# Performance work log

Measured on AMD Instinct MI355X. Metric: run time of the kernel, lower is better.

## Reference

```python
import jax, jax.numpy as jnp
import numpy as np

SCALES = (8, 16, 32)  # matches init kwarg scale=[8,16,32]


def _pairwise_dist(x):
    # Euclidean cdist via the norm trick; clamp for numerical safety.
    sq = jnp.sum(x * x, axis=1)
    d2 = sq[:, None] + sq[None, :] - 2.0 * (x @ x.T)
    return jnp.sqrt(jnp.maximum(d2, 0.0))


def setup_inputs() -> dict:
    key = jax.random.key(0)
    k1, k2 = jax.random.split(key)
    N, D = 8192, 256
    feats_c_norm = jax.random.normal(k1, (N, D), dtype=jnp.float32)
    point_c_norm = jax.random.normal(k2, (N, 3), dtype=jnp.float32)
    f_masks = jnp.ones((N,), dtype=bool)  # all valid -> masked gather is identity (static shapes)
    return {"feats_c_norm": feats_c_norm, "point_c_norm": point_c_norm, "f_masks": f_masks}


def reference(feats_c_norm, point_c_norm, f_masks):
    # f_masks is all-True here, so feats_c_norm[f_indices] == feats_c_norm (identity).
    N = feats_c_norm.shape[0]
    dists = _pairwise_dist(point_c_norm)                     # [N, N]
    kmax = min(max(SCALES), N - 1) + 1
    # top_k of -dists gives the kmax smallest distances, sorted ascending,
    # so slicing idx[:, 1:s+1] reproduces per-scale topk(largest=False) exactly.
    _, idx = jax.lax.top_k(-dists, kmax)                     # [N, kmax] int32
    outs = [feats_c_norm]                                    # key 0 in the original dict
    for s in SCALES:
        s = min(s, N - 1)
        neighbor_feats = feats_c_norm[idx[:, 1:s + 1]]       # [N, s, D]
        outs.append(neighbor_feats.reshape(N, -1))           # [N, s*D]
    return tuple(outs)
```

## Files before the change

### kernel.cpp

```cpp
#include <hip/hip_runtime.h>

#define NPTS 8192
#define KSEL 33
#define SCAP 512

typedef float vf4 __attribute__((ext_vector_type(4)));

__global__ __launch_bounds__(256) void prep_kernel(const float* __restrict__ pts,
                                                   float4* __restrict__ pts4) {
#pragma clang fp contract(off)
    const int j = blockIdx.x * 256 + threadIdx.x;
    const float x = pts[j * 3 + 0];
    const float y = pts[j * 3 + 1];
    const float z = pts[j * 3 + 2];
    const float sq = (x * x + y * y) + z * z;
    pts4[j] = make_float4(x, y, z, sq);
}

__global__ __launch_bounds__(256, 4) void knn_fused_kernel(const float4* __restrict__ pts4,
                                                           const float* __restrict__ feats,
                                                           float* __restrict__ out) {
#pragma clang fp contract(off)
    const int i = blockIdx.x;
    const int tid = threadIdx.x;
    const int lane = tid & 63;
    const int wv = tid >> 6;

    __shared__ unsigned red[4];
    __shared__ int sh_cnt;
    __shared__ unsigned long long S[SCAP];
    __shared__ unsigned jlist[32];

    const float4 pi = pts4[i];

    unsigned d[32];
    unsigned m1 = 0xFFFFFFFFu, m2 = 0xFFFFFFFFu;
#pragma unroll
    for (int t = 0; t < 32; ++t) {
        const int j = tid + t * 256;
        const float4 pj = pts4[j];
        const float dot = __builtin_fmaf(pi.z, pj.z, __builtin_fmaf(pi.y, pj.y, pi.x * pj.x));
        const float d2 = (pi.w + pj.w) - (2.0f * dot);
        const unsigned db = __float_as_uint(fmaxf(d2, 0.0f));
        d[t] = db;
        const unsigned mx = db > m1 ? db : m1;
        m1 = db < m1 ? db : m1;
        m2 = mx < m2 ? mx : m2;
    }
    if (tid == 0) sh_cnt = 0;

    unsigned blo = 0u, bhi = 0x7F800000u;
    while (blo < bhi) {
        const unsigned mid = (blo + bhi) >> 1;
        const int cnt = __popcll(__ballot(m1 <= mid)) + __popcll(__ballot(m2 <= mid));
        if (cnt >= KSEL) bhi = mid; else blo = mid + 1u;
    }
    if (lane == 0) red[wv] = bhi;
    __syncthreads();
    unsigned T = red[0];
    T = red[1] < T ? red[1] : T;
    T = red[2] < T ? red[2] : T;
    T = red[3] < T ? red[3] : T;

    const float s = sqrtf(__uint_as_float(T));
    const float snx = __uint_as_float(__float_as_uint(s) + 1u);
    const unsigned T2 = __float_as_uint(__fmul_rn(snx, snx)) + 2u;

    int n = 0;
#pragma unroll
    for (int t = 0; t < 32; ++t) n += (d[t] <= T2) ? 1 : 0;

    int incl = n;
#pragma unroll
    for (int sh = 1; sh < 64; sh <<= 1) {
        const int o = __shfl_up(incl, sh, 64);
        if (lane >= sh) incl += o;
    }
    int base = 0;
    if (lane == 63) base = atomicAdd(&sh_cnt, incl);
    base = __shfl(base, 63, 64);
    int ptr = base + incl - n;
#pragma unroll
    for (int t = 0; t < 32; ++t) {
        if (d[t] <= T2) {
            const unsigned db = __float_as_uint(sqrtf(__uint_as_float(d[t])));
            if (ptr < SCAP)
                S[ptr] = (((unsigned long long)db) << 32) | (unsigned)(tid + t * 256);
            ++ptr;
        }
    }
    __syncthreads();

    const int c = sh_cnt < SCAP ? sh_cnt : SCAP;
    for (int q = tid; q < c; q += 256) {
        const unsigned long long key = S[q];
        int rank = 0;
        for (int u = 0; u < c; ++u) rank += (S[u] < key) ? 1 : 0;
        if (rank >= 1 && rank < KSEL) jlist[rank - 1] = (unsigned)key;
    }
    __syncthreads();

    const unsigned long long O1 = (unsigned long long)NPTS * 256ull;
    const unsigned long long O2 = O1 + (unsigned long long)NPTS * 2048ull;
    const unsigned long long O3 = O2 + (unsigned long long)NPTS * 4096ull;
    const unsigned long long ii = (unsigned long long)i;

    vf4 vself;
    if (wv == 0) {
        const vf4* sp = (const vf4*)(feats + ii * 256ull);
        vself = sp[lane];
    }
    vf4 vk[8];
    unsigned kk[8];
#pragma unroll
    for (int m = 0; m < 8; ++m) {
        const int k = wv + 4 * m;
        const unsigned src = jlist[k];
        kk[m] = (unsigned)k;
        const vf4* sp = (const vf4*)(feats + (unsigned long long)src * 256ull);
        vk[m] = sp[lane];
    }

    if (wv == 0) {
        __builtin_nontemporal_store(vself, &((vf4*)(out + ii * 256ull))[lane]);
    }
#pragma unroll
    for (int m = 0; m < 8; ++m) {
        const unsigned k = kk[m];
        const vf4 v = vk[m];
        __builtin_nontemporal_store(v,
            &((vf4*)(out + O3 + ii * 8192ull + (unsigned long long)k * 256ull))[lane]);
        if (k < 16u)
            __builtin_nontemporal_store(v,
                &((vf4*)(out + O2 + ii * 4096ull + (unsigned long long)k * 256ull))[lane]);
        if (k < 8u)
            __builtin_nontemporal_store(v,
                &((vf4*)(out + O1 + ii * 2048ull + (unsigned long long)k * 256ull))[lane]);
    }
}

extern "C" void kernel_launch(void* const* d_in, const int* in_sizes, int n_in,
                              void* d_out, int out_size, void* d_ws, size_t ws_size,
                              hipStream_t stream) {
    const float* feats = (const float*)d_in[0];
    const float* pts = (const float*)d_in[1];

    float4* pts4 = (float4*)d_ws;

    prep_kernel<<<NPTS / 256, 256, 0, stream>>>(pts, pts4);
    knn_fused_kernel<<<NPTS, 256, 0, stream>>>(pts4, feats, (float*)d_out);
}
```

Measured before the change: 176.8 us.

## Use 512-thread blocks with 16 points per thread in fused kNN kernel

Result: faster. 172.2 us (-2.6%).

```diff
diff --git a/kernel.cpp b/kernel.cpp
--- a/kernel.cpp
+++ b/kernel.cpp
@@ -2,7 +2,9 @@
 
 #define NPTS 8192
 #define KSEL 33
-#define SCAP 512
+#define TPB  512
+#define TSL  16
+#define SCAP 1024
 
 typedef float vf4 __attribute__((ext_vector_type(4)));
 
@@ -17,27 +19,34 @@
     pts4[j] = make_float4(x, y, z, sq);
 }
 
-__global__ __launch_bounds__(256, 4) void knn_fused_kernel(const float4* __restrict__ pts4,
-                                                           const float* __restrict__ feats,
-                                                           float* __restrict__ out) {
+__global__ __launch_bounds__(TPB) void knn_fused_kernel(const float4* __restrict__ pts4,
+                                                        const float* __restrict__ feats,
+                                                        float* __restrict__ out) {
 #pragma clang fp contract(off)
     const int i = blockIdx.x;
     const int tid = threadIdx.x;
     const int lane = tid & 63;
     const int wv = tid >> 6;
 
-    __shared__ unsigned red[4];
+    __shared__ unsigned red[8];
     __shared__ int sh_cnt;
     __shared__ unsigned long long S[SCAP];
     __shared__ unsigned jlist[32];
 
     const float4 pi = pts4[i];
+    const unsigned long long ii = (unsigned long long)i;
 
-    unsigned d[32];
+    vf4 vself;
+    if (wv == 0) {
+        const vf4* sp = (const vf4*)(feats + ii * 256ull);
+        vself = sp[lane];
+    }
+
+    unsigned d[TSL];
     unsigned m1 = 0xFFFFFFFFu, m2 = 0xFFFFFFFFu;
 #pragma unroll
-    for (int t = 0; t < 32; ++t) {
-        const int j = tid + t * 256;
+    for (int t = 0; t < TSL; ++t) {
+        const int j = tid + t * TPB;
         const float4 pj = pts4[j];
         const float dot = __builtin_fmaf(pi.z, pj.z, __builtin_fmaf(pi.y, pj.y, pi.x * pj.x));
         const float d2 = (pi.w + pj.w) - (2.0f * dot);
@@ -46,6 +55,7 @@
         const unsigned mx = db > m1 ? db : m1;
         m1 = db < m1 ? db : m1;
         m2 = mx < m2 ? mx : m2;
+        if ((t & 3) == 3) __builtin_amdgcn_sched_barrier(0);
     }
     if (tid == 0) sh_cnt = 0;
 
@@ -58,9 +68,8 @@
     if (lane == 0) red[wv] = bhi;
     __syncthreads();
     unsigned T = red[0];
-    T = red[1] < T ? red[1] : T;
-    T = red[2] < T ? red[2] : T;
-    T = red[3] < T ? red[3] : T;
+#pragma unroll
+    for (int w = 1; w < 8; ++w) T = red[w] < T ? red[w] : T;
 
     const float s = sqrtf(__uint_as_float(T));
     const float snx = __uint_as_float(__float_as_uint(s) + 1u);
@@ -68,7 +77,7 @@
 
     int n = 0;
 #pragma unroll
-    for (int t = 0; t < 32; ++t) n += (d[t] <= T2) ? 1 : 0;
+    for (int t = 0; t < TSL; ++t) n += (d[t] <= T2) ? 1 : 0;
 
     int incl = n;
 #pragma unroll
@@ -81,18 +90,18 @@
     base = __shfl(base, 63, 64);
     int ptr = base + incl - n;
 #pragma unroll
-    for (int t = 0; t < 32; ++t) {
+    for (int t = 0; t < TSL; ++t) {
         if (d[t] <= T2) {
             const unsigned db = __float_as_uint(sqrtf(__uint_as_float(d[t])));
             if (ptr < SCAP)
-                S[ptr] = (((unsigned long long)db) << 32) | (unsigned)(tid + t * 256);
+                S[ptr] = (((unsigned long long)db) << 32) | (unsigned)(tid + t * TPB);
             ++ptr;
         }
     }
     __syncthreads();
 
     const int c = sh_cnt < SCAP ? sh_cnt : SCAP;
-    for (int q = tid; q < c; q += 256) {
+    for (int q = tid; q < c; q += TPB) {
         const unsigned long long key = S[q];
         int rank = 0;
         for (int u = 0; u < c; ++u) rank += (S[u] < key) ? 1 : 0;
@@ -103,20 +112,11 @@
     const unsigned long long O1 = (unsigned long long)NPTS * 256ull;
     const unsigned long long O2 = O1 + (unsigned long long)NPTS * 2048ull;
     const unsigned long long O3 = O2 + (unsigned long long)NPTS * 4096ull;
-    const unsigned long long ii = (unsigned long long)i;
 
-    vf4 vself;
-    if (wv == 0) {
-        const vf4* sp = (const vf4*)(feats + ii * 256ull);
-        vself = sp[lane];
-    }
-    vf4 vk[8];
-    unsigned kk[8];
+    vf4 vk[4];
 #pragma unroll
-    for (int m = 0; m < 8; ++m) {
-        const int k = wv + 4 * m;
-        const unsigned src = jlist[k];
-        kk[m] = (unsigned)k;
+    for (int m = 0; m < 4; ++m) {
+        const unsigned src = jlist[wv + 8 * m];
         const vf4* sp = (const vf4*)(feats + (unsigned long long)src * 256ull);
         vk[m] = sp[lane];
     }
@@ -125,8 +125,8 @@
         __builtin_nontemporal_store(vself, &((vf4*)(out + ii * 256ull))[lane]);
     }
 #pragma unroll
-    for (int m = 0; m < 8; ++m) {
-        const unsigned k = kk[m];
+    for (int m = 0; m < 4; ++m) {
+        const unsigned k = (unsigned)(wv + 8 * m);
         const vf4 v = vk[m];
         __builtin_nontemporal_store(v,
             &((vf4*)(out + O3 + ii * 8192ull + (unsigned long long)k * 256ull))[lane]);
@@ -148,5 +148,5 @@
     float4* pts4 = (float4*)d_ws;
 
     prep_kernel<<<NPTS / 256, 256, 0, stream>>>(pts, pts4);
-    knn_fused_kernel<<<NPTS, 256, 0, stream>>>(pts4, feats, (float*)d_out);
+    knn_fused_kernel<<<NPTS, TPB, 0, stream>>>(pts4, feats, (float*)d_out);
 }
```
